# Kernel optimization log

Hardware: AMD Instinct MI355X
Metric: run time of the kernel (lower is better)

The kernel has to match this reference:

```python
import jax, jax.numpy as jnp
from jax import lax
import numpy as np

B, N, NPOINT, NSAMPLE = 16, 4096, 1024, 32
RADIUS = 0.2
D_FEAT = 64
IN_CH = 3 + D_FEAT
MLP = (64, 64, 128)
EPS = 1e-5


def fps(xyz, npoint):
    # farthest point sampling, xyz: [B,N,3] -> idx [B,npoint] (start at index 0)
    Bn, Nn, _ = xyz.shape
    batch = jnp.arange(Bn)

    def step(carry, _):
        dist, far = carry                      # dist [B,N], far [B]
        centroid = xyz[batch, far]             # [B,3]
        d = jnp.sum((xyz - centroid[:, None, :]) ** 2, -1)
        dist = jnp.minimum(dist, d)
        new_far = jnp.argmax(dist, -1).astype(jnp.int32)
        return (dist, new_far), far

    init = (jnp.full((Bn, Nn), 1e10, xyz.dtype), jnp.zeros((Bn,), jnp.int32))
    _, idxs = lax.scan(step, init, None, length=npoint)
    return jnp.transpose(idxs)                 # [B, npoint]


def square_distance(a, b):
    # a [B,S,3], b [B,N,3] -> [B,S,N]
    return (jnp.sum(a * a, -1)[:, :, None]
            + jnp.sum(b * b, -1)[:, None, :]
            - 2.0 * jnp.einsum('bsc,bnc->bsn', a, b))


def query_ball(radius, nsample, xyz, new_xyz):
    Nn = xyz.shape[1]
    sqr = square_distance(new_xyz, xyz)                      # [B,S,N]
    gi = jnp.where(sqr > radius ** 2, Nn, jnp.arange(Nn, dtype=jnp.int32))
    gi = jnp.sort(gi, axis=-1)[:, :, :nsample]               # [B,S,K]
    first = gi[:, :, :1]
    return jnp.where(gi == Nn, first, gi)


def gather_points(pts, idx):
    # pts [B,N,C], idx [B,...] -> [B,...,C]
    return jax.vmap(lambda p, i: p[i])(pts, idx)


def _forward(xyz, points, params):
    x = jnp.transpose(xyz, (0, 2, 1))          # [B,N,3]
    p = jnp.transpose(points, (0, 2, 1))       # [B,N,D]
    fidx = fps(x, NPOINT)                      # [B,S]
    new_xyz = gather_points(x, fidx)           # [B,S,3]
    idx = query_ball(RADIUS, NSAMPLE, x, new_xyz)  # [B,S,K]
    g_xyz = gather_points(x, idx)              # [B,S,K,3]
    g_norm = g_xyz - new_xyz[:, :, None, :]
    g_pts = gather_points(p, idx)              # [B,S,K,D]
    feat = jnp.concatenate([g_norm, g_pts], -1)  # [B,S,K,3+D]
    h = jnp.transpose(feat, (0, 3, 2, 1))      # [B,C,K,S]
    for (w, b, g, bt) in params:
        h = jnp.einsum('bcks,oc->boks', h, w) + b[None, :, None, None]
        m = jnp.mean(h, axis=(0, 2, 3), keepdims=True)
        v = jnp.mean((h - m) ** 2, axis=(0, 2, 3), keepdims=True)  # biased var (train BN)
        h = g[None, :, None, None] * (h - m) * lax.rsqrt(v + EPS) + bt[None, :, None, None]
        h = jax.nn.relu(h)
    new_points = jnp.max(h, axis=2)            # [B,Cout,S]
    return jnp.transpose(new_xyz, (0, 2, 1)), new_points


def setup_inputs() -> dict:
    key = jax.random.key(0)
    ks = jax.random.split(key, 16)
    xyz = jax.random.uniform(ks[0], (B, 3, N), dtype=jnp.float32)
    points = jax.random.normal(ks[1], (B, D_FEAT, N), dtype=jnp.float32)
    inp = {'xyz': xyz, 'points': points}
    cin = IN_CH
    for l, cout in enumerate(MLP):
        scale = 1.0 / np.sqrt(cin)
        inp[f'w{l}'] = jax.random.normal(ks[2 + 4 * l], (cout, cin), dtype=jnp.float32) * scale
        inp[f'b{l}'] = jax.random.normal(ks[3 + 4 * l], (cout,), dtype=jnp.float32) * scale
        inp[f'g{l}'] = jnp.ones((cout,), jnp.float32)
        inp[f'bt{l}'] = jnp.zeros((cout,), jnp.float32)
        cin = cout
    return inp


def reference(xyz, points, w0, b0, g0, bt0, w1, b1, g1, bt1, w2, b2, g2, bt2):
    params = [(w0, b0, g0, bt0), (w1, b1, g1, bt1), (w2, b2, g2, bt2)]
    return _forward(xyz, points, params)
```

## Files before the change

### kernel.cpp

```cpp
#include <hip/hip_runtime.h>
#include <stdint.h>

#define NB    16
#define NN    4096
#define NP    1024
#define NS    32
#define NGRP  (NB*NP)
#define CNT   524288.0
#define NWRK  240

typedef short  bf16x8 __attribute__((ext_vector_type(8)));
typedef float  f32x4  __attribute__((ext_vector_type(4)));

__device__ __forceinline__ float bf2f(unsigned short u) {
    return __uint_as_float(((unsigned)u) << 16);
}
__device__ __forceinline__ unsigned short f2bf(float f) {
    unsigned u = __float_as_uint(f);
    unsigned r = u + 0x7fffu + ((u >> 16) & 1u);
    return (unsigned short)(r >> 16);
}
__device__ __forceinline__ bf16x8 as_bf(uint4 u) {
    union { uint4 a; bf16x8 b; } c; c.a = u; return c.b;
}

template <int CTRL, int RM>
__device__ __forceinline__ unsigned long long dppmax(unsigned long long k) {
    int lo = (int)(unsigned)k;
    int hi = (int)(k >> 32);
    int ml = __builtin_amdgcn_update_dpp(lo, lo, CTRL, RM, 0xf, false);
    int mh = __builtin_amdgcn_update_dpp(hi, hi, CTRL, RM, 0xf, false);
    unsigned long long m = ((unsigned long long)(unsigned)mh << 32) | (unsigned)ml;
    return m > k ? m : k;
}

__global__ __launch_bounds__(256, 1) void fused_kernel(const float* __restrict__ xyz,
                                                       const float* __restrict__ points,
                                                       const float* __restrict__ w0,
                                                       const float* __restrict__ b0,
                                                       int* __restrict__ fidx,
                                                       unsigned short* __restrict__ T,
                                                       int* __restrict__ idx,
                                                       double* __restrict__ stage1,
                                                       float* __restrict__ out0,
                                                       int* __restrict__ sync_ctr) {
    __shared__ float4 sxyz4[NN];
    __shared__ unsigned long long red[2][4];
    __shared__ int fbuf[NP];
    __shared__ int gidx[4][NS];
    int tid = threadIdx.x;
    int wv = tid >> 6, lane = tid & 63;

    if (blockIdx.x < 16) {
        int b = blockIdx.x;
        const float* xb = xyz + (size_t)b * 3 * NN;
        float px[16], py[16], pz[16], dist[16];
#pragma unroll
        for (int i = 0; i < 16; i++) {
            int n = i * 256 + tid;
            px[i] = xb[n]; py[i] = xb[NN + n]; pz[i] = xb[2 * NN + n];
            sxyz4[n] = make_float4(px[i], py[i], pz[i], 0.f);
            dist[i] = 1e10f;
        }
#pragma unroll
        for (int i = 0; i < 16; i++) {
            asm volatile("" : "+v"(px[i]));
            asm volatile("" : "+v"(py[i]));
            asm volatile("" : "+v"(pz[i]));
        }
        int far = 0;
        if (tid == 0) fbuf[0] = 0;
        __syncthreads();
        for (int t = 0; t < NP; t++) {
            float4 c = sxyz4[far];
            float cx = c.x, cy = c.y, cz = c.z;
            float bv = -1.0f; int bi = 0;
#pragma unroll
            for (int i = 0; i < 16; i++) {
                float dx = __fsub_rn(px[i], cx);
                float dy = __fsub_rn(py[i], cy);
                float dz = __fsub_rn(pz[i], cz);
                float d = __fadd_rn(__fadd_rn(__fmul_rn(dx, dx), __fmul_rn(dy, dy)),
                                    __fmul_rn(dz, dz));
                float nd = fminf(dist[i], d);
                dist[i] = nd;
                if (nd > bv) { bv = nd; bi = i; }
            }
            int n_best = bi * 256 + tid;
            unsigned long long k =
                ((unsigned long long)__float_as_uint(bv) << 32) |
                (unsigned long long)(~(unsigned)n_best);
            k = dppmax<0x111, 0xf>(k);
            k = dppmax<0x112, 0xf>(k);
            k = dppmax<0x114, 0xf>(k);
            k = dppmax<0x118, 0xf>(k);
            k = dppmax<0x142, 0xa>(k);
            k = dppmax<0x143, 0xc>(k);
            if ((tid & 63) == 63) red[t & 1][wv] = k;
            asm volatile("s_waitcnt lgkmcnt(0)\n\ts_barrier" ::: "memory");
            if ((t & 15) == 15 && tid < 16) {
                int i = (t - 15) + tid;
                __hip_atomic_store(&fidx[b * NP + i], fbuf[i],
                                   __ATOMIC_RELAXED, __HIP_MEMORY_SCOPE_AGENT);
            }
            ulonglong2 ra = *(ulonglong2*)&red[t & 1][0];
            ulonglong2 rb = *(ulonglong2*)&red[t & 1][2];
            unsigned long long r0 = ra.x, r1 = ra.y, r2 = rb.x, r3 = rb.y;
            if (r1 > r0) r0 = r1;
            if (r3 > r2) r2 = r3;
            if (r2 > r0) r0 = r2;
            far = (int)(~(unsigned)r0);
            if (tid == 0 && t + 1 < NP) fbuf[t + 1] = far;
        }
        return;
    }

    int w = blockIdx.x - 16;
    for (int j = 0; j < 2; j++) {
        int gid = w * 256 + tid + j * (NWRK * 256);
        if (gid < NB * NN) {
            int b = gid >> 12, n = gid & (NN - 1);
            const float* xb = xyz + (size_t)b * 3 * NN;
            const float* pb = points + (size_t)b * 64 * NN;
            float acc[64];
#pragma unroll
            for (int o = 0; o < 64; o++) acc[o] = 0.f;
            for (int c = 0; c < 67; c++) {
                float v = (c < 3) ? xb[c * NN + n] : pb[(c - 3) * NN + n];
#pragma unroll
                for (int o = 0; o < 64; o++) acc[o] = fmaf(v, w0[o * 67 + c], acc[o]);
            }
            unsigned short* dst = T + (size_t)gid * 64;
            for (int oo = 0; oo < 64; oo += 8) {
                union { unsigned short u[8]; uint4 v; } r;
#pragma unroll
                for (int jj = 0; jj < 8; jj++) r.u[jj] = f2bf(acc[oo + jj]);
                *(uint4*)&dst[oo] = r.v;
            }
        }
    }
    __syncthreads();
    __threadfence();
    if (tid == 0) {
        __hip_atomic_fetch_add(sync_ctr, 1, __ATOMIC_ACQ_REL, __HIP_MEMORY_SCOPE_AGENT);
        while (__hip_atomic_load(sync_ctr, __ATOMIC_ACQUIRE, __HIP_MEMORY_SCOPE_AGENT) < NWRK)
            __builtin_amdgcn_s_sleep(32);
    }
    __syncthreads();
    __threadfence();

    {
        int b = w & 15;
        int r = w >> 4;
        const float* xb = xyz + (size_t)b * 3 * NN;
        const unsigned short* Tb = T + (size_t)b * NN * 64;
        for (int kk = r; kk < 256; kk += 15) {
            int s = (kk << 2) + wv;
            int g = (b << 10) + s;
            int fid;
            if (lane == 0) {
                fid = __hip_atomic_load(&fidx[g], __ATOMIC_RELAXED, __HIP_MEMORY_SCOPE_AGENT);
                while (fid < 0) {
                    __builtin_amdgcn_s_sleep(16);
                    fid = __hip_atomic_load(&fidx[g], __ATOMIC_RELAXED, __HIP_MEMORY_SCOPE_AGENT);
                }
            }
            fid = __shfl(fid, 0);
            float cx = xb[fid], cy = xb[NN + fid], cz = xb[2 * NN + fid];
            if (lane < 3) {
                float v = (lane == 0) ? cx : ((lane == 1) ? cy : cz);
                out0[((size_t)b * 3 + lane) * NP + s] = v;
            }
            float sa = __fadd_rn(__fadd_rn(__fmul_rn(cx, cx), __fmul_rn(cy, cy)),
                                 __fmul_rn(cz, cz));
            int* out = idx + (size_t)g * NS;
            int total = 0; int first = 0;
            for (int ci = 0; ci < NN / 64; ci++) {
                int n = ci * 64 + lane;
                float x = xb[n], y = xb[NN + n], z = xb[2 * NN + n];
                float sb = __fadd_rn(__fadd_rn(__fmul_rn(x, x), __fmul_rn(y, y)),
                                     __fmul_rn(z, z));
                float dot = __fadd_rn(__fadd_rn(__fmul_rn(x, cx), __fmul_rn(y, cy)),
                                      __fmul_rn(z, cz));
                float sqr = __fsub_rn(__fadd_rn(sa, sb), __fmul_rn(2.0f, dot));
                bool pred = !(sqr > 0.04f);
                unsigned long long mask = __ballot(pred);
                if (mask) {
                    if (total == 0) first = ci * 64 + (int)__builtin_ctzll(mask);
                    int pos = total + (int)__popcll(mask & ((1ull << lane) - 1ull));
                    if (pred && pos < NS) { out[pos] = n; gidx[wv][pos] = n; }
                    total += (int)__popcll(mask);
                    if (total >= NS) break;
                }
            }
            if (total < NS) {
                if (lane >= total && lane < NS) { out[lane] = first; gidx[wv][lane] = first; }
            }
            int o = lane;
            float uo = fmaf(w0[o * 67 + 2], cz, fmaf(w0[o * 67 + 1], cy, w0[o * 67] * cx));
            float bo = b0[o];
            float s1 = 0.f, s2 = 0.f;
            for (int k = 0; k < NS; k++) {
                int n = gidx[wv][k];
                float tv = bf2f(Tb[(size_t)n * 64 + o]);
                float h = tv - uo + bo;
                s1 += h; s2 = fmaf(h, h, s2);
            }
            int slot = g & 63;
            atomicAdd(&stage1[slot * 128 + o], (double)s1);
            atomicAdd(&stage1[slot * 128 + 64 + o], (double)s2);
        }
    }
}

__global__ void finalize_kernel(const double* __restrict__ stage, int C,
                                const float* __restrict__ gamma,
                                const float* __restrict__ beta,
                                float* __restrict__ AB) {
    int o = threadIdx.x;
    double s = 0.0, q = 0.0;
    for (int i = 0; i < 64; i++) {
        s += stage[i * 2 * C + o];
        q += stage[i * 2 * C + C + o];
    }
    double m = s * (1.0 / CNT);
    double v = q * (1.0 / CNT) - m * m;
    double A = (double)gamma[o] / sqrt(v + 1e-5);
    AB[o] = (float)A;
    AB[C + o] = (float)((double)beta[o] - m * A);
}

__global__ __launch_bounds__(256) void layer2_kernel(const float* __restrict__ xyz,
                                                     const unsigned short* __restrict__ T,
                                                     const int* __restrict__ fidx,
                                                     const int* __restrict__ idx,
                                                     const float* __restrict__ w0,
                                                     const float* __restrict__ b0,
                                                     const float* __restrict__ AB1,
                                                     const float* __restrict__ w1,
                                                     const float* __restrict__ b1,
                                                     unsigned short* __restrict__ h2,
                                                     double* __restrict__ stage2) {
    __shared__ __attribute__((aligned(16))) unsigned short w1s[64][72];
    __shared__ __attribute__((aligned(16))) unsigned short h1s[4][32][72];
    __shared__ float psum[64], psq[64];
    int t = threadIdx.x, wv = t >> 6, lane = t & 63;
    int quad = lane >> 4, col = lane & 15;
    int g = blockIdx.x * 4 + wv;
    int b = g >> 10;
    for (int lin = t; lin < 4096; lin += 256)
        w1s[lin >> 6][lin & 63] = f2bf(w1[lin]);
    if (t < 64) { psum[t] = 0.f; psq[t] = 0.f; }
    {
        int fid = fidx[g];
        const float* xb = xyz + (size_t)b * 3 * NN;
        float cx = xb[fid], cy = xb[NN + fid], cz = xb[2 * NN + fid];
        int o = lane;
        float uo = fmaf(w0[o * 67 + 2], cz, fmaf(w0[o * 67 + 1], cy, w0[o * 67] * cx));
        float bo = b0[o];
        float a1 = AB1[o], bb1 = AB1[64 + o];
        const int* gi = idx + (size_t)g * NS;
        const unsigned short* Tb = T + (size_t)b * NN * 64;
        for (int k = 0; k < NS; k++) {
            int n = gi[k];
            float tv = bf2f(Tb[(size_t)n * 64 + o]);
            float h = tv - uo + bo;
            float hn = fmaxf(fmaf(h, a1, bb1), 0.f);
            h1s[wv][k][o] = f2bf(hn);
        }
    }
    __syncthreads();
    f32x4 acc[2][4];
#pragma unroll
    for (int i = 0; i < 2; i++)
#pragma unroll
        for (int j = 0; j < 4; j++) acc[i][j] = (f32x4){0.f, 0.f, 0.f, 0.f};
#pragma unroll
    for (int ks = 0; ks < 2; ks++) {
        bf16x8 a0 = as_bf(*(const uint4*)&h1s[wv][col][ks * 32 + quad * 8]);
        bf16x8 a1f = as_bf(*(const uint4*)&h1s[wv][16 + col][ks * 32 + quad * 8]);
#pragma unroll
        for (int nt = 0; nt < 4; nt++) {
            bf16x8 bf = as_bf(*(const uint4*)&w1s[nt * 16 + col][ks * 32 + quad * 8]);
            acc[0][nt] = __builtin_amdgcn_mfma_f32_16x16x32_bf16(a0, bf, acc[0][nt], 0, 0, 0);
            acc[1][nt] = __builtin_amdgcn_mfma_f32_16x16x32_bf16(a1f, bf, acc[1][nt], 0, 0, 0);
        }
    }
    float s1[4], s2[4];
#pragma unroll
    for (int nt = 0; nt < 4; nt++) {
        float bb = b1[nt * 16 + col];
        s1[nt] = 0.f; s2[nt] = 0.f;
#pragma unroll
        for (int mt = 0; mt < 2; mt++)
#pragma unroll
            for (int r = 0; r < 4; r++) {
                float v = acc[mt][nt][r] + bb;
                s1[nt] += v; s2[nt] = fmaf(v, v, s2[nt]);
                h1s[wv][mt * 16 + quad * 4 + r][nt * 16 + col] = f2bf(v);
            }
        s1[nt] += __shfl_xor(s1[nt], 16); s1[nt] += __shfl_xor(s1[nt], 32);
        s2[nt] += __shfl_xor(s2[nt], 16); s2[nt] += __shfl_xor(s2[nt], 32);
        if (quad == 0) {
            atomicAdd(&psum[nt * 16 + col], s1[nt]);
            atomicAdd(&psq[nt * 16 + col], s2[nt]);
        }
    }
#pragma unroll
    for (int r = 0; r < 4; r++) {
        int lin = lane + 64 * r;
        int row = lin >> 3, c = lin & 7;
        uint4 v = *(const uint4*)&h1s[wv][row][c * 8];
        *(uint4*)&h2[((size_t)g * NS + row) * 64 + c * 8] = v;
    }
    __syncthreads();
    if (t < 64) {
        int slot = blockIdx.x & 63;
        atomicAdd(&stage2[slot * 128 + t], (double)psum[t]);
        atomicAdd(&stage2[slot * 128 + 64 + t], (double)psq[t]);
    }
}

__global__ __launch_bounds__(256) void layer3_kernel(const unsigned short* __restrict__ h2,
                                                     const float* __restrict__ AB2,
                                                     const float* __restrict__ w2,
                                                     const float* __restrict__ b2,
                                                     double* __restrict__ stage3,
                                                     float* __restrict__ mxbuf,
                                                     float* __restrict__ mnbuf) {
    __shared__ __attribute__((aligned(16))) unsigned short w2s[128][72];
    __shared__ __attribute__((aligned(16))) unsigned short h2s[4][32][72];
    __shared__ float psum[128], psq[128];
    int t = threadIdx.x, wv = t >> 6, lane = t & 63;
    int quad = lane >> 4, col = lane & 15;
    int g = blockIdx.x * 4 + wv;
    for (int lin = t; lin < 8192; lin += 256)
        w2s[lin >> 6][lin & 63] = f2bf(w2[lin]);
    if (t < 128) { psum[t] = 0.f; psq[t] = 0.f; }
    {
        int c = lane & 7;
        float a2v[8], bb2v[8];
#pragma unroll
        for (int j = 0; j < 8; j++) {
            a2v[j] = AB2[c * 8 + j];
            bb2v[j] = AB2[64 + c * 8 + j];
        }
        const unsigned short* hg = h2 + (size_t)g * NS * 64;
#pragma unroll
        for (int r = 0; r < 4; r++) {
            int row = (lane >> 3) + 8 * r;
            union { uint4 v; unsigned short u[8]; } in, outp;
            in.v = *(const uint4*)&hg[row * 64 + c * 8];
#pragma unroll
            for (int j = 0; j < 8; j++) {
                float f = bf2f(in.u[j]);
                outp.u[j] = f2bf(fmaxf(fmaf(f, a2v[j], bb2v[j]), 0.f));
            }
            *(uint4*)&h2s[wv][row][c * 8] = outp.v;
        }
    }
    __syncthreads();
    f32x4 acc[2][8];
#pragma unroll
    for (int i = 0; i < 2; i++)
#pragma unroll
        for (int j = 0; j < 8; j++) acc[i][j] = (f32x4){0.f, 0.f, 0.f, 0.f};
#pragma unroll
    for (int ks = 0; ks < 2; ks++) {
        bf16x8 a0 = as_bf(*(const uint4*)&h2s[wv][col][ks * 32 + quad * 8]);
        bf16x8 a1f = as_bf(*(const uint4*)&h2s[wv][16 + col][ks * 32 + quad * 8]);
#pragma unroll
        for (int nt = 0; nt < 8; nt++) {
            bf16x8 bf = as_bf(*(const uint4*)&w2s[nt * 16 + col][ks * 32 + quad * 8]);
            acc[0][nt] = __builtin_amdgcn_mfma_f32_16x16x32_bf16(a0, bf, acc[0][nt], 0, 0, 0);
            acc[1][nt] = __builtin_amdgcn_mfma_f32_16x16x32_bf16(a1f, bf, acc[1][nt], 0, 0, 0);
        }
    }
#pragma unroll
    for (int nt = 0; nt < 8; nt++) {
        float bb = b2[nt * 16 + col];
        float s1 = 0.f, s2 = 0.f, mx = -1e30f, mn = 1e30f;
#pragma unroll
        for (int mt = 0; mt < 2; mt++)
#pragma unroll
            for (int r = 0; r < 4; r++) {
                float v = acc[mt][nt][r] + bb;
                s1 += v; s2 = fmaf(v, v, s2);
                mx = fmaxf(mx, v); mn = fminf(mn, v);
            }
        s1 += __shfl_xor(s1, 16); s1 += __shfl_xor(s1, 32);
        s2 += __shfl_xor(s2, 16); s2 += __shfl_xor(s2, 32);
        mx = fmaxf(mx, __shfl_xor(mx, 16)); mx = fmaxf(mx, __shfl_xor(mx, 32));
        mn = fminf(mn, __shfl_xor(mn, 16)); mn = fminf(mn, __shfl_xor(mn, 32));
        if (quad == 0) {
            atomicAdd(&psum[nt * 16 + col], s1);
            atomicAdd(&psq[nt * 16 + col], s2);
            mxbuf[(size_t)g * 128 + nt * 16 + col] = mx;
            mnbuf[(size_t)g * 128 + nt * 16 + col] = mn;
        }
    }
    __syncthreads();
    if (t < 128) {
        int slot = blockIdx.x & 63;
        atomicAdd(&stage3[slot * 256 + t], (double)psum[t]);
        atomicAdd(&stage3[slot * 256 + 128 + t], (double)psq[t]);
    }
}

__global__ __launch_bounds__(256) void epilogue_kernel(const float* __restrict__ mxbuf,
                                                       const float* __restrict__ mnbuf,
                                                       const float* __restrict__ AB3,
                                                       float* __restrict__ out1) {
    __shared__ float tile[32][65];
    int blk = blockIdx.x;
    int b = blk >> 6; int rem = blk & 63;
    int o0 = (rem >> 4) * 32; int s0 = (rem & 15) * 64;
    int t = threadIdx.x;
#pragma unroll
    for (int j = 0; j < 8; j++) {
        int lin = t + 256 * j;
        int sl = lin >> 5, ol = lin & 31;
        int o = o0 + ol;
        float a = AB3[o], bb = AB3[128 + o];
        size_t src = ((size_t)b * NP + s0 + sl) * 128 + o;
        float v = (a >= 0.f) ? mxbuf[src] : mnbuf[src];
        tile[ol][sl] = fmaxf(fmaf(v, a, bb), 0.f);
    }
    __syncthreads();
#pragma unroll
    for (int j = 0; j < 8; j++) {
        int lin = t + 256 * j;
        int ol = lin >> 6, sl = lin & 63;
        out1[((size_t)b * 128 + o0 + ol) * NP + s0 + sl] = tile[ol][sl];
    }
}

extern "C" void kernel_launch(void* const* d_in, const int* in_sizes, int n_in,
                              void* d_out, int out_size, void* d_ws, size_t ws_size,
                              hipStream_t stream) {
    const float* xyz    = (const float*)d_in[0];
    const float* points = (const float*)d_in[1];
    const float* w0  = (const float*)d_in[2];
    const float* b0  = (const float*)d_in[3];
    const float* g0  = (const float*)d_in[4];
    const float* bt0 = (const float*)d_in[5];
    const float* w1  = (const float*)d_in[6];
    const float* b1  = (const float*)d_in[7];
    const float* g1  = (const float*)d_in[8];
    const float* bt1 = (const float*)d_in[9];
    const float* w2  = (const float*)d_in[10];
    const float* b2  = (const float*)d_in[11];
    const float* g2  = (const float*)d_in[12];
    const float* bt2 = (const float*)d_in[13];

    char* ws = (char*)d_ws;
    int*            fidx = (int*)(ws + 0);
    int*            idx  = (int*)(ws + 65536);
    unsigned short* T    = (unsigned short*)(ws + 2162688);
    unsigned short* h2   = (unsigned short*)(ws + 10551296);
    float*          mxbuf = (float*)(ws + 77660160);
    float*          mnbuf = (float*)(ws + 86048768);
    double*         stage = (double*)(ws + 94437376);
    float*          AB   = (float*)(ws + 94699520);
    int*            sync_ctr = (int*)(ws + 94701312);
    double* stage1 = stage;
    double* stage2 = stage + 64 * 128;
    double* stage3 = stage + 2 * 64 * 128;
    float* AB1 = AB; float* AB2 = AB + 128; float* AB3 = AB + 256;
    float* out0 = (float*)d_out;
    float* out1 = out0 + NB * 3 * NP;

    hipMemsetAsync(stage, 0, 262144, stream);
    hipMemsetAsync(fidx, 0xFF, NB * NP * 4, stream);
    hipMemsetAsync(sync_ctr, 0, 4, stream);

    fused_kernel<<<256, 256, 0, stream>>>(xyz, points, w0, b0, fidx, T, idx,
                                          stage1, out0, sync_ctr);
    finalize_kernel<<<1, 64, 0, stream>>>(stage1, 64, g0, bt0, AB1);
    layer2_kernel<<<NGRP / 4, 256, 0, stream>>>(xyz, T, fidx, idx, w0, b0, AB1,
                                                w1, b1, h2, stage2);
    finalize_kernel<<<1, 64, 0, stream>>>(stage2, 64, g1, bt1, AB2);
    layer3_kernel<<<NGRP / 4, 256, 0, stream>>>(h2, AB2, w2, b2, stage3, mxbuf, mnbuf);
    finalize_kernel<<<1, 128, 0, stream>>>(stage3, 128, g2, bt2, AB3);
    epilogue_kernel<<<1024, 256, 0, stream>>>(mxbuf, mnbuf, AB3, out1);
}
```

Before: 825.7 us.

## Fuse BN finalize, layer2, layer3 and epilogue into one persistent kernel

Replaces six kernel launches (three finalize, layer2, layer3, epilogue) with one persistent 1024-block kernel that loops over groups and uses software grid barriers between layers. Each block recomputes the BN scale and shift itself, and the weights are loaded into shared memory once per block rather than once per 4 groups. This removes launch gaps and the tiny single-block finalize kernels. In exchange it relies on all 1024 blocks being co-resident for the spin barrier (launch_bounds 256,4), and the barrier itself adds spinning cost.

```diff
diff --git a/kernel.cpp b/kernel.cpp
--- a/kernel.cpp
+++ b/kernel.cpp
@@ -8,6 +8,7 @@
 #define NGRP  (NB*NP)
 #define CNT   524288.0
 #define NWRK  240
+#define TGRID 1024
 
 typedef short  bf16x8 __attribute__((ext_vector_type(8)));
 typedef float  f32x4  __attribute__((ext_vector_type(4)));
@@ -213,225 +214,263 @@
     }
 }
 
-__global__ void finalize_kernel(const double* __restrict__ stage, int C,
-                                const float* __restrict__ gamma,
-                                const float* __restrict__ beta,
-                                float* __restrict__ AB) {
-    int o = threadIdx.x;
-    double s = 0.0, q = 0.0;
-    for (int i = 0; i < 64; i++) {
-        s += stage[i * 2 * C + o];
-        q += stage[i * 2 * C + C + o];
-    }
-    double m = s * (1.0 / CNT);
-    double v = q * (1.0 / CNT) - m * m;
-    double A = (double)gamma[o] / sqrt(v + 1e-5);
-    AB[o] = (float)A;
-    AB[C + o] = (float)((double)beta[o] - m * A);
-}
-
-__global__ __launch_bounds__(256) void layer2_kernel(const float* __restrict__ xyz,
-                                                     const unsigned short* __restrict__ T,
-                                                     const int* __restrict__ fidx,
-                                                     const int* __restrict__ idx,
-                                                     const float* __restrict__ w0,
-                                                     const float* __restrict__ b0,
-                                                     const float* __restrict__ AB1,
-                                                     const float* __restrict__ w1,
-                                                     const float* __restrict__ b1,
-                                                     unsigned short* __restrict__ h2,
-                                                     double* __restrict__ stage2) {
-    __shared__ __attribute__((aligned(16))) unsigned short w1s[64][72];
-    __shared__ __attribute__((aligned(16))) unsigned short h1s[4][32][72];
-    __shared__ float psum[64], psq[64];
+__global__ __launch_bounds__(256, 4) void tail_kernel(
+        const float* __restrict__ xyz, const unsigned short* __restrict__ T,
+        const int* __restrict__ fidx, const int* __restrict__ idx,
+        const float* __restrict__ w0, const float* __restrict__ b0,
+        const double* __restrict__ stage1, const float* __restrict__ g0v, const float* __restrict__ bt0v,
+        const float* __restrict__ w1, const float* __restrict__ b1,
+        double* __restrict__ stage2, const float* __restrict__ g1v, const float* __restrict__ bt1v,
+        const float* __restrict__ w2, const float* __restrict__ b2,
+        double* __restrict__ stage3, const float* __restrict__ g2v, const float* __restrict__ bt2v,
+        unsigned short* __restrict__ h2, float* __restrict__ mxbuf, float* __restrict__ mnbuf,
+        float* __restrict__ out1, int* __restrict__ bar_ctr, int* __restrict__ bar_gen) {
+    __shared__ union {
+        struct { unsigned short w1s[64][72]; unsigned short h1s[4][32][72]; } A;
+        struct { unsigned short w2s[128][72]; unsigned short h2s[4][32][72]; } B;
+        struct { float tile[128][17]; } C;
+    } sm;
+    __shared__ float psum[128], psq[128];
+    __shared__ float ab1[128], ab2[128], ab3[256];
     int t = threadIdx.x, wv = t >> 6, lane = t & 63;
     int quad = lane >> 4, col = lane & 15;
-    int g = blockIdx.x * 4 + wv;
-    int b = g >> 10;
+    int blk = blockIdx.x;
+
+    if (t < 64) {
+        double s = 0.0, q = 0.0;
+        for (int i = 0; i < 64; i++) { s += stage1[i * 128 + t]; q += stage1[i * 128 + 64 + t]; }
+        double m = s * (1.0 / CNT);
+        double v = q * (1.0 / CNT) - m * m;
+        double A = (double)g0v[t] / sqrt(v + 1e-5);
+        ab1[t] = (float)A;
+        ab1[64 + t] = (float)((double)bt0v[t] - m * A);
+    }
     for (int lin = t; lin < 4096; lin += 256)
-        w1s[lin >> 6][lin & 63] = f2bf(w1[lin]);
-    if (t < 64) { psum[t] = 0.f; psq[t] = 0.f; }
+        sm.A.w1s[lin >> 6][lin & 63] = f2bf(w1[lin]);
+    __syncthreads();
+
+    for (int it = 0; it < 4; it++) {
+        int qq = blk * 4 + it;
+        int g = qq * 4 + wv;
+        int b = g >> 10;
+        if (t < 64) { psum[t] = 0.f; psq[t] = 0.f; }
+        {
+            int fid = fidx[g];
+            const float* xb = xyz + (size_t)b * 3 * NN;
+            float cx = xb[fid], cy = xb[NN + fid], cz = xb[2 * NN + fid];
+            int o = lane;
+            float uo = fmaf(w0[o * 67 + 2], cz, fmaf(w0[o * 67 + 1], cy, w0[o * 67] * cx));
+            float bo = b0[o];
+            float a1 = ab1[o], bb1 = ab1[64 + o];
+            const int* gi = idx + (size_t)g * NS;
+            const unsigned short* Tb = T + (size_t)b * NN * 64;
+            for (int k = 0; k < NS; k++) {
+                int n = gi[k];
+                float tv = bf2f(Tb[(size_t)n * 64 + o]);
+                float h = tv - uo + bo;
+                float hn = fmaxf(fmaf(h, a1, bb1), 0.f);
+                sm.A.h1s[wv][k][o] = f2bf(hn);
+            }
+        }
+        __syncthreads();
+        f32x4 acc[2][4];
+#pragma unroll
+        for (int i = 0; i < 2; i++)
+#pragma unroll
+            for (int j = 0; j < 4; j++) acc[i][j] = (f32x4){0.f, 0.f, 0.f, 0.f};
+#pragma unroll
+        for (int ks = 0; ks < 2; ks++) {
+            bf16x8 a0 = as_bf(*(const uint4*)&sm.A.h1s[wv][col][ks * 32 + quad * 8]);
+            bf16x8 a1f = as_bf(*(const uint4*)&sm.A.h1s[wv][16 + col][ks * 32 + quad * 8]);
+#pragma unroll
+            for (int nt = 0; nt < 4; nt++) {
+                bf16x8 bf = as_bf(*(const uint4*)&sm.A.w1s[nt * 16 + col][ks * 32 + quad * 8]);
+                acc[0][nt] = __builtin_amdgcn_mfma_f32_16x16x32_bf16(a0, bf, acc[0][nt], 0, 0, 0);
+                acc[1][nt] = __builtin_amdgcn_mfma_f32_16x16x32_bf16(a1f, bf, acc[1][nt], 0, 0, 0);
+            }
+        }
+        float s1[4], s2[4];
+#pragma unroll
+        for (int nt = 0; nt < 4; nt++) {
+            float bb = b1[nt * 16 + col];
+            s1[nt] = 0.f; s2[nt] = 0.f;
+#pragma unroll
+            for (int mt = 0; mt < 2; mt++)
+#pragma unroll
+                for (int r = 0; r < 4; r++) {
+                    float v = acc[mt][nt][r] + bb;
+                    s1[nt] += v; s2[nt] = fmaf(v, v, s2[nt]);
+                    sm.A.h1s[wv][mt * 16 + quad * 4 + r][nt * 16 + col] = f2bf(v);
+                }
+            s1[nt] += __shfl_xor(s1[nt], 16); s1[nt] += __shfl_xor(s1[nt], 32);
+            s2[nt] += __shfl_xor(s2[nt], 16); s2[nt] += __shfl_xor(s2[nt], 32);
+            if (quad == 0) {
+                atomicAdd(&psum[nt * 16 + col], s1[nt]);
+                atomicAdd(&psq[nt * 16 + col], s2[nt]);
+            }
+        }
+#pragma unroll
+        for (int r = 0; r < 4; r++) {
+            int lin = lane + 64 * r;
+            int row = lin >> 3, c = lin & 7;
+            uint4 v = *(const uint4*)&sm.A.h1s[wv][row][c * 8];
+            *(uint4*)&h2[((size_t)g * NS + row) * 64 + c * 8] = v;
+        }
+        __syncthreads();
+        if (t < 64) {
+            int slot = qq & 63;
+            atomicAdd(&stage2[slot * 128 + t], (double)psum[t]);
+            atomicAdd(&stage2[slot * 128 + 64 + t], (double)psq[t]);
+        }
+        __syncthreads();
+    }
+
+    __syncthreads();
+    __threadfence();
+    if (t == 0) {
+        int n = __hip_atomic_fetch_add(bar_ctr, 1, __ATOMIC_ACQ_REL, __HIP_MEMORY_SCOPE_AGENT);
+        if (n == TGRID - 1) {
+            __hip_atomic_store(bar_ctr, 0, __ATOMIC_RELAXED, __HIP_MEMORY_SCOPE_AGENT);
+            __hip_atomic_store(bar_gen, 1, __ATOMIC_RELEASE, __HIP_MEMORY_SCOPE_AGENT);
+        } else {
+            while (__hip_atomic_load(bar_gen, __ATOMIC_ACQUIRE, __HIP_MEMORY_SCOPE_AGENT) < 1)
+                __builtin_amdgcn_s_sleep(8);
+        }
+    }
+    __syncthreads();
+    __threadfence();
+
+    if (t < 64) {
+        double s = 0.0, q = 0.0;
+        for (int i = 0; i < 64; i++) { s += stage2[i * 128 + t]; q += stage2[i * 128 + 64 + t]; }
+        double m = s * (1.0 / CNT);
+        double v = q * (1.0 / CNT) - m * m;
+        double A = (double)g1v[t] / sqrt(v + 1e-5);
+        ab2[t] = (float)A;
+        ab2[64 + t] = (float)((double)bt1v[t] - m * A);
+    }
+    for (int lin = t; lin < 8192; lin += 256)
+        sm.B.w2s[lin >> 6][lin & 63] = f2bf(w2[lin]);
+    __syncthreads();
+
+    for (int it = 0; it < 4; it++) {
+        int qq = blk * 4 + it;
+        int g = qq * 4 + wv;
+        if (t < 128) { psum[t] = 0.f; psq[t] = 0.f; }
+        {
+            int c = lane & 7;
+            float a2v[8], bb2v[8];
+#pragma unroll
+            for (int j = 0; j < 8; j++) {
+                a2v[j] = ab2[c * 8 + j];
+                bb2v[j] = ab2[64 + c * 8 + j];
+            }
+            const unsigned short* hg = h2 + (size_t)g * NS * 64;
+#pragma unroll
+            for (int r = 0; r < 4; r++) {
+                int row = (lane >> 3) + 8 * r;
+                union { uint4 v; unsigned short u[8]; } in, outp;
+                in.v = *(const uint4*)&hg[row * 64 + c * 8];
+#pragma unroll
+                for (int j = 0; j < 8; j++) {
+                    float f = bf2f(in.u[j]);
+                    outp.u[j] = f2bf(fmaxf(fmaf(f, a2v[j], bb2v[j]), 0.f));
+                }
+                *(uint4*)&sm.B.h2s[wv][row][c * 8] = outp.v;
+            }
+        }
+        __syncthreads();
+        f32x4 acc[2][8];
+#pragma unroll
+        for (int i = 0; i < 2; i++)
+#pragma unroll
+            for (int j = 0; j < 8; j++) acc[i][j] = (f32x4){0.f, 0.f, 0.f, 0.f};
+#pragma unroll
+        for (int ks = 0; ks < 2; ks++) {
+            bf16x8 a0 = as_bf(*(const uint4*)&sm.B.h2s[wv][col][ks * 32 + quad * 8]);
+            bf16x8 a1f = as_bf(*(const uint4*)&sm.B.h2s[wv][16 + col][ks * 32 + quad * 8]);
+#pragma unroll
+            for (int nt = 0; nt < 8; nt++) {
+                bf16x8 bf = as_bf(*(const uint4*)&sm.B.w2s[nt * 16 + col][ks * 32 + quad * 8]);
+                acc[0][nt] = __builtin_amdgcn_mfma_f32_16x16x32_bf16(a0, bf, acc[0][nt], 0, 0, 0);
+                acc[1][nt] = __builtin_amdgcn_mfma_f32_16x16x32_bf16(a1f, bf, acc[1][nt], 0, 0, 0);
+            }
+        }
+#pragma unroll
+        for (int nt = 0; nt < 8; nt++) {
+            float bb = b2[nt * 16 + col];
+            float s1 = 0.f, s2 = 0.f, mx = -1e30f, mn = 1e30f;
+#pragma unroll
+            for (int mt = 0; mt < 2; mt++)
+#pragma unroll
+                for (int r = 0; r < 4; r++) {
+                    float v = acc[mt][nt][r] + bb;
+                    s1 += v; s2 = fmaf(v, v, s2);
+                    mx = fmaxf(mx, v); mn = fminf(mn, v);
+                }
+            s1 += __shfl_xor(s1, 16); s1 += __shfl_xor(s1, 32);
+            s2 += __shfl_xor(s2, 16); s2 += __shfl_xor(s2, 32);
+            mx = fmaxf(mx, __shfl_xor(mx, 16)); mx = fmaxf(mx, __shfl_xor(mx, 32));
+            mn = fminf(mn, __shfl_xor(mn, 16)); mn = fminf(mn, __shfl_xor(mn, 32));
+            if (quad == 0) {
+                atomicAdd(&psum[nt * 16 + col], s1);
+                atomicAdd(&psq[nt * 16 + col], s2);
+                mxbuf[(size_t)g * 128 + nt * 16 + col] = mx;
+                mnbuf[(size_t)g * 128 + nt * 16 + col] = mn;
+            }
+        }
+        __syncthreads();
+        if (t < 128) {
+            int slot = qq & 63;
+            atomicAdd(&stage3[slot * 256 + t], (double)psum[t]);
+            atomicAdd(&stage3[slot * 256 + 128 + t], (double)psq[t]);
+        }
+        __syncthreads();
+    }
+
+    __syncthreads();
+    __threadfence();
+    if (t == 0) {
+        int n = __hip_atomic_fetch_add(bar_ctr, 1, __ATOMIC_ACQ_REL, __HIP_MEMORY_SCOPE_AGENT);
+        if (n == TGRID - 1) {
+            __hip_atomic_store(bar_ctr, 0, __ATOMIC_RELAXED, __HIP_MEMORY_SCOPE_AGENT);
+            __hip_atomic_store(bar_gen, 2, __ATOMIC_RELEASE, __HIP_MEMORY_SCOPE_AGENT);
+        } else {
+            while (__hip_atomic_load(bar_gen, __ATOMIC_ACQUIRE, __HIP_MEMORY_SCOPE_AGENT) < 2)
+                __builtin_amdgcn_s_sleep(8);
+        }
+    }
+    __syncthreads();
+    __threadfence();
+
+    if (t < 128) {
+        double s = 0.0, q = 0.0;
+        for (int i = 0; i < 64; i++) { s += stage3[i * 256 + t]; q += stage3[i * 256 + 128 + t]; }
+        double m = s * (1.0 / CNT);
+        double v = q * (1.0 / CNT) - m * m;
+        double A = (double)g2v[t] / sqrt(v + 1e-5);
+        ab3[t] = (float)A;
+        ab3[128 + t] = (float)((double)bt2v[t] - m * A);
+    }
+    __syncthreads();
+
     {
-        int fid = fidx[g];
-        const float* xb = xyz + (size_t)b * 3 * NN;
-        float cx = xb[fid], cy = xb[NN + fid], cz = xb[2 * NN + fid];
-        int o = lane;
-        float uo = fmaf(w0[o * 67 + 2], cz, fmaf(w0[o * 67 + 1], cy, w0[o * 67] * cx));
-        float bo = b0[o];
-        float a1 = AB1[o], bb1 = AB1[64 + o];
-        const int* gi = idx + (size_t)g * NS;
-        const unsigned short* Tb = T + (size_t)b * NN * 64;
-        for (int k = 0; k < NS; k++) {
-            int n = gi[k];
-            float tv = bf2f(Tb[(size_t)n * 64 + o]);
-            float h = tv - uo + bo;
-            float hn = fmaxf(fmaf(h, a1, bb1), 0.f);
-            h1s[wv][k][o] = f2bf(hn);
-        }
-    }
-    __syncthreads();
-    f32x4 acc[2][4];
-#pragma unroll
-    for (int i = 0; i < 2; i++)
-#pragma unroll
-        for (int j = 0; j < 4; j++) acc[i][j] = (f32x4){0.f, 0.f, 0.f, 0.f};
-#pragma unroll
-    for (int ks = 0; ks < 2; ks++) {
-        bf16x8 a0 = as_bf(*(const uint4*)&h1s[wv][col][ks * 32 + quad * 8]);
-        bf16x8 a1f = as_bf(*(const uint4*)&h1s[wv][16 + col][ks * 32 + quad * 8]);
-#pragma unroll
-        for (int nt = 0; nt < 4; nt++) {
-            bf16x8 bf = as_bf(*(const uint4*)&w1s[nt * 16 + col][ks * 32 + quad * 8]);
-            acc[0][nt] = __builtin_amdgcn_mfma_f32_16x16x32_bf16(a0, bf, acc[0][nt], 0, 0, 0);
-            acc[1][nt] = __builtin_amdgcn_mfma_f32_16x16x32_bf16(a1f, bf, acc[1][nt], 0, 0, 0);
-        }
-    }
-    float s1[4], s2[4];
-#pragma unroll
-    for (int nt = 0; nt < 4; nt++) {
-        float bb = b1[nt * 16 + col];
-        s1[nt] = 0.f; s2[nt] = 0.f;
-#pragma unroll
-        for (int mt = 0; mt < 2; mt++)
-#pragma unroll
-            for (int r = 0; r < 4; r++) {
-                float v = acc[mt][nt][r] + bb;
-                s1[nt] += v; s2[nt] = fmaf(v, v, s2[nt]);
-                h1s[wv][mt * 16 + quad * 4 + r][nt * 16 + col] = f2bf(v);
-            }
-        s1[nt] += __shfl_xor(s1[nt], 16); s1[nt] += __shfl_xor(s1[nt], 32);
-        s2[nt] += __shfl_xor(s2[nt], 16); s2[nt] += __shfl_xor(s2[nt], 32);
-        if (quad == 0) {
-            atomicAdd(&psum[nt * 16 + col], s1[nt]);
-            atomicAdd(&psq[nt * 16 + col], s2[nt]);
-        }
-    }
-#pragma unroll
-    for (int r = 0; r < 4; r++) {
-        int lin = lane + 64 * r;
-        int row = lin >> 3, c = lin & 7;
-        uint4 v = *(const uint4*)&h1s[wv][row][c * 8];
-        *(uint4*)&h2[((size_t)g * NS + row) * 64 + c * 8] = v;
-    }
-    __syncthreads();
-    if (t < 64) {
-        int slot = blockIdx.x & 63;
-        atomicAdd(&stage2[slot * 128 + t], (double)psum[t]);
-        atomicAdd(&stage2[slot * 128 + 64 + t], (double)psq[t]);
-    }
-}
-
-__global__ __launch_bounds__(256) void layer3_kernel(const unsigned short* __restrict__ h2,
-                                                     const float* __restrict__ AB2,
-                                                     const float* __restrict__ w2,
-                                                     const float* __restrict__ b2,
-                                                     double* __restrict__ stage3,
-                                                     float* __restrict__ mxbuf,
-                                                     float* __restrict__ mnbuf) {
-    __shared__ __attribute__((aligned(16))) unsigned short w2s[128][72];
-    __shared__ __attribute__((aligned(16))) unsigned short h2s[4][32][72];
-    __shared__ float psum[128], psq[128];
-    int t = threadIdx.x, wv = t >> 6, lane = t & 63;
-    int quad = lane >> 4, col = lane & 15;
-    int g = blockIdx.x * 4 + wv;
-    for (int lin = t; lin < 8192; lin += 256)
-        w2s[lin >> 6][lin & 63] = f2bf(w2[lin]);
-    if (t < 128) { psum[t] = 0.f; psq[t] = 0.f; }
-    {
-        int c = lane & 7;
-        float a2v[8], bb2v[8];
-#pragma unroll
+        int gbase = blk * 16;
+        int b = gbase >> 10, s0 = gbase & 1023;
         for (int j = 0; j < 8; j++) {
-            a2v[j] = AB2[c * 8 + j];
-            bb2v[j] = AB2[64 + c * 8 + j];
-        }
-        const unsigned short* hg = h2 + (size_t)g * NS * 64;
-#pragma unroll
-        for (int r = 0; r < 4; r++) {
-            int row = (lane >> 3) + 8 * r;
-            union { uint4 v; unsigned short u[8]; } in, outp;
-            in.v = *(const uint4*)&hg[row * 64 + c * 8];
-#pragma unroll
-            for (int j = 0; j < 8; j++) {
-                float f = bf2f(in.u[j]);
-                outp.u[j] = f2bf(fmaxf(fmaf(f, a2v[j], bb2v[j]), 0.f));
-            }
-            *(uint4*)&h2s[wv][row][c * 8] = outp.v;
-        }
-    }
-    __syncthreads();
-    f32x4 acc[2][8];
-#pragma unroll
-    for (int i = 0; i < 2; i++)
-#pragma unroll
-        for (int j = 0; j < 8; j++) acc[i][j] = (f32x4){0.f, 0.f, 0.f, 0.f};
-#pragma unroll
-    for (int ks = 0; ks < 2; ks++) {
-        bf16x8 a0 = as_bf(*(const uint4*)&h2s[wv][col][ks * 32 + quad * 8]);
-        bf16x8 a1f = as_bf(*(const uint4*)&h2s[wv][16 + col][ks * 32 + quad * 8]);
-#pragma unroll
-        for (int nt = 0; nt < 8; nt++) {
-            bf16x8 bf = as_bf(*(const uint4*)&w2s[nt * 16 + col][ks * 32 + quad * 8]);
-            acc[0][nt] = __builtin_amdgcn_mfma_f32_16x16x32_bf16(a0, bf, acc[0][nt], 0, 0, 0);
-            acc[1][nt] = __builtin_amdgcn_mfma_f32_16x16x32_bf16(a1f, bf, acc[1][nt], 0, 0, 0);
-        }
-    }
-#pragma unroll
-    for (int nt = 0; nt < 8; nt++) {
-        float bb = b2[nt * 16 + col];
-        float s1 = 0.f, s2 = 0.f, mx = -1e30f, mn = 1e30f;
-#pragma unroll
-        for (int mt = 0; mt < 2; mt++)
-#pragma unroll
-            for (int r = 0; r < 4; r++) {
-                float v = acc[mt][nt][r] + bb;
-                s1 += v; s2 = fmaf(v, v, s2);
-                mx = fmaxf(mx, v); mn = fminf(mn, v);
-            }
-        s1 += __shfl_xor(s1, 16); s1 += __shfl_xor(s1, 32);
-        s2 += __shfl_xor(s2, 16); s2 += __shfl_xor(s2, 32);
-        mx = fmaxf(mx, __shfl_xor(mx, 16)); mx = fmaxf(mx, __shfl_xor(mx, 32));
-        mn = fminf(mn, __shfl_xor(mn, 16)); mn = fminf(mn, __shfl_xor(mn, 32));
-        if (quad == 0) {
-            atomicAdd(&psum[nt * 16 + col], s1);
-            atomicAdd(&psq[nt * 16 + col], s2);
-            mxbuf[(size_t)g * 128 + nt * 16 + col] = mx;
-            mnbuf[(size_t)g * 128 + nt * 16 + col] = mn;
-        }
-    }
-    __syncthreads();
-    if (t < 128) {
-        int slot = blockIdx.x & 63;
-        atomicAdd(&stage3[slot * 256 + t], (double)psum[t]);
-        atomicAdd(&stage3[slot * 256 + 128 + t], (double)psq[t]);
-    }
-}
-
-__global__ __launch_bounds__(256) void epilogue_kernel(const float* __restrict__ mxbuf,
-                                                       const float* __restrict__ mnbuf,
-                                                       const float* __restrict__ AB3,
-                                                       float* __restrict__ out1) {
-    __shared__ float tile[32][65];
-    int blk = blockIdx.x;
-    int b = blk >> 6; int rem = blk & 63;
-    int o0 = (rem >> 4) * 32; int s0 = (rem & 15) * 64;
-    int t = threadIdx.x;
-#pragma unroll
-    for (int j = 0; j < 8; j++) {
-        int lin = t + 256 * j;
-        int sl = lin >> 5, ol = lin & 31;
-        int o = o0 + ol;
-        float a = AB3[o], bb = AB3[128 + o];
-        size_t src = ((size_t)b * NP + s0 + sl) * 128 + o;
-        float v = (a >= 0.f) ? mxbuf[src] : mnbuf[src];
-        tile[ol][sl] = fmaxf(fmaf(v, a, bb), 0.f);
-    }
-    __syncthreads();
-#pragma unroll
-    for (int j = 0; j < 8; j++) {
-        int lin = t + 256 * j;
-        int ol = lin >> 6, sl = lin & 63;
-        out1[((size_t)b * 128 + o0 + ol) * NP + s0 + sl] = tile[ol][sl];
+            int lin = t + 256 * j;
+            int sl = lin >> 7, o = lin & 127;
+            float a = ab3[o], bb = ab3[128 + o];
+            size_t src = (size_t)(gbase + sl) * 128 + o;
+            float v = (a >= 0.f) ? mxbuf[src] : mnbuf[src];
+            sm.C.tile[o][sl] = fmaxf(fmaf(v, a, bb), 0.f);
+        }
+        __syncthreads();
+        for (int j = 0; j < 8; j++) {
+            int lin = t + 256 * j;
+            int o = lin >> 4, sl = lin & 15;
+            out1[((size_t)b * 128 + o) * NP + s0 + sl] = sm.C.tile[o][sl];
+        }
     }
 }
 
@@ -461,26 +500,25 @@
     float*          mxbuf = (float*)(ws + 77660160);
     float*          mnbuf = (float*)(ws + 86048768);
     double*         stage = (double*)(ws + 94437376);
-    float*          AB   = (float*)(ws + 94699520);
     int*            sync_ctr = (int*)(ws + 94701312);
+    int*            bar_ctr  = (int*)(ws + 94701316);
+    int*            bar_gen  = (int*)(ws + 94701320);
     double* stage1 = stage;
     double* stage2 = stage + 64 * 128;
     double* stage3 = stage + 2 * 64 * 128;
-    float* AB1 = AB; float* AB2 = AB + 128; float* AB3 = AB + 256;
     float* out0 = (float*)d_out;
     float* out1 = out0 + NB * 3 * NP;
 
     hipMemsetAsync(stage, 0, 262144, stream);
     hipMemsetAsync(fidx, 0xFF, NB * NP * 4, stream);
-    hipMemsetAsync(sync_ctr, 0, 4, stream);
+    hipMemsetAsync(sync_ctr, 0, 12, stream);
 
     fused_kernel<<<256, 256, 0, stream>>>(xyz, points, w0, b0, fidx, T, idx,
                                           stage1, out0, sync_ctr);
-    finalize_kernel<<<1, 64, 0, stream>>>(stage1, 64, g0, bt0, AB1);
-    layer2_kernel<<<NGRP / 4, 256, 0, stream>>>(xyz, T, fidx, idx, w0, b0, AB1,
-                                                w1, b1, h2, stage2);
-    finalize_kernel<<<1, 64, 0, stream>>>(stage2, 64, g1, bt1, AB2);
-    layer3_kernel<<<NGRP / 4, 256, 0, stream>>>(h2, AB2, w2, b2, stage3, mxbuf, mnbuf);
-    finalize_kernel<<<1, 128, 0, stream>>>(stage3, 128, g2, bt2, AB3);
-    epilogue_kernel<<<1024, 256, 0, stream>>>(mxbuf, mnbuf, AB3, out1);
-}
+    tail_kernel<<<TGRID, 256, 0, stream>>>(xyz, T, fidx, idx, w0, b0,
+                                           stage1, g0, bt0,
+                                           w1, b1, stage2, g1, bt1,
+                                           w2, b2, stage3, g2, bt2,
+                                           h2, mxbuf, mnbuf, out1,
+                                           bar_ctr, bar_gen);
+}
```

Result: slower. 1.445 ms (+75.0%).
